# Kernel tuning notes

Measured on AMD Instinct MI355X. Metric: run time of the kernel, lower is better.

The kernel has to match this reference:

```python
import jax, jax.numpy as jnp
import numpy as np

SIZE = 1024      # codebook size
DIM = 64         # latent_dim
TOPK = 3
BETA_C = 0.25
LEGACY = False

def setup_inputs() -> dict:
    key = jax.random.key(0)
    kz, ke = jax.random.split(key)
    z = jax.random.normal(kz, (16, 64, 64, DIM), dtype=jnp.float32)
    # nn.Embedding init: uniform(-1/size, 1/size)
    emb = jax.random.uniform(ke, (SIZE, DIM), minval=-1.0 / SIZE, maxval=1.0 / SIZE, dtype=jnp.float32)
    return {"z": z, "emb": emb}

def reference(z, emb):
    zf = z.reshape(-1, DIM)                                  # [N, D]
    # squared euclidean distances via matmul expansion: [N, SIZE]
    d = (jnp.sum(zf ** 2, axis=1, keepdims=True)
         + jnp.sum(emb ** 2, axis=1)
         - 2.0 * (zf @ emb.T))
    neg_d, topk_idx = jax.lax.top_k(-d, TOPK)                # smallest distances -> [N, K]
    # direct gather instead of one-hot matmul (same math)
    z_q = jnp.mean(emb[topk_idx], axis=1).reshape(z.shape)   # [N,K,D] -> [N,D] -> z.shape
    if LEGACY:
        loss = (jnp.mean((jax.lax.stop_gradient(z_q) - z) ** 2)
                + BETA_C * jnp.mean((z_q - jax.lax.stop_gradient(z)) ** 2))
    else:
        loss = (BETA_C * jnp.mean((jax.lax.stop_gradient(z_q) - z) ** 2)
                + jnp.mean((z_q - jax.lax.stop_gradient(z)) ** 2))
    # one-hot encodings are part of the module's return signature
    topk_encodings = jax.nn.one_hot(topk_idx, SIZE, dtype=z.dtype)   # [N, K, SIZE]
    e_mean = jnp.mean(topk_encodings, axis=(0, 1))                   # [SIZE]
    perplexity = jnp.exp(-jnp.sum(e_mean * jnp.log(e_mean + 1e-10)))
    z_q_st = z + jax.lax.stop_gradient(z_q - z)              # straight-through estimator
    return (z_q_st, loss, perplexity, topk_encodings, topk_idx)
```

## Files before the change

### kernel.cpp

```cpp
#include <hip/hip_runtime.h>
#include <math.h>

#define N_ROWS 65536
#define CB 1024
#define SPLITS 4
#define JS (CB / SPLITS)

typedef float v4f __attribute__((ext_vector_type(4)));

__device__ __forceinline__ float tree_sum64_sq(const float* x) {
#pragma clang fp contract(off)
    float sq[64];
#pragma unroll
    for (int i = 0; i < 64; ++i) sq[i] = x[i] * x[i];
    float s[16];
#pragma unroll
    for (int l = 0; l < 16; ++l) s[l] = (sq[l] + sq[l + 16]) + (sq[l + 32] + sq[l + 48]);
    float t[8];
#pragma unroll
    for (int l = 0; l < 8; ++l) t[l] = s[l] + s[l + 8];
    float u[4];
#pragma unroll
    for (int l = 0; l < 4; ++l) u[l] = t[l] + t[l + 4];
    float v0 = u[0] + u[2];
    float v1 = u[1] + u[3];
    return v0 + v1;
}

__device__ __forceinline__ void top3_insert(float d, int j,
                                            float& v0, float& v1, float& v2,
                                            int& i0, int& i1, int& i2) {
    bool b0 = d < v0, b1 = d < v1, b2 = d < v2;
    v2 = b1 ? v1 : (b2 ? d : v2);
    i2 = b1 ? i1 : (b2 ? j : i2);
    v1 = b0 ? v0 : (b1 ? d : v1);
    i1 = b0 ? i0 : (b1 ? j : i1);
    v0 = b0 ? d : v0;
    i0 = b0 ? j : i0;
}

__global__ __launch_bounds__(256) void prep_kernel(const float* __restrict__ emb,
                                                   float* __restrict__ B,
                                                   int* __restrict__ hist,
                                                   float* __restrict__ lossAcc) {
    int j = blockIdx.x * 256 + threadIdx.x;
    if (j >= CB) return;
    float e[64];
    const float4* e4 = (const float4*)(emb + (size_t)j * 64);
#pragma unroll
    for (int k = 0; k < 16; ++k) {
        float4 v = e4[k];
        e[4 * k] = v.x; e[4 * k + 1] = v.y; e[4 * k + 2] = v.z; e[4 * k + 3] = v.w;
    }
    B[j] = tree_sum64_sq(e);
    hist[j] = 0;
    if (j == 0) *lossAcc = 0.0f;
}

__global__ __launch_bounds__(256) void fused_kernel(const float* __restrict__ z,
                                                    const float* __restrict__ emb,
                                                    const float* __restrict__ B,
                                                    float* __restrict__ out0,
                                                    float* __restrict__ out4,
                                                    int* __restrict__ hist,
                                                    float* __restrict__ lossAcc) {
    __shared__ float sD[SPLITS][64][3];
    __shared__ int   sI[SPLITS][64][3];

    int t = threadIdx.x;
    int r = t & 63;
    int split = __builtin_amdgcn_readfirstlane(t >> 6);
    int row = blockIdx.x * 64 + r;

    float zr[64];
    const float4* z4 = (const float4*)(z + (size_t)row * 64);
#pragma unroll
    for (int k = 0; k < 16; ++k) {
        float4 v = z4[k];
        zr[4 * k] = v.x; zr[4 * k + 1] = v.y; zr[4 * k + 2] = v.z; zr[4 * k + 3] = v.w;
    }
    float A = tree_sum64_sq(zr);

    float v0 = 3.402823466e38f, v1 = 3.402823466e38f, v2 = 3.402823466e38f;
    int i0 = 0, i1 = 0, i2 = 0;
    int jbase = split * JS;

    for (int jj = 0; jj < JS; ++jj) {
        int j = jbase + jj;
        const float4* e4 = (const float4*)(emb + (size_t)j * 64);
        float Bj = B[j];
        float acc = 0.0f;
#pragma unroll
        for (int k = 0; k < 16; ++k) {
            float4 e = e4[k];
            acc = fmaf(zr[4 * k],     e.x, acc);
            acc = fmaf(zr[4 * k + 1], e.y, acc);
            acc = fmaf(zr[4 * k + 2], e.z, acc);
            acc = fmaf(zr[4 * k + 3], e.w, acc);
        }
        float d = (A + Bj) - 2.0f * acc;
        top3_insert(d, j, v0, v1, v2, i0, i1, i2);
    }

    sD[split][r][0] = v0; sD[split][r][1] = v1; sD[split][r][2] = v2;
    sI[split][r][0] = i0; sI[split][r][1] = i1; sI[split][r][2] = i2;
    __syncthreads();

    if (t < 64) {
        float m0 = 3.402823466e38f, m1 = 3.402823466e38f, m2 = 3.402823466e38f;
        int j0 = 0, j1 = 0, j2 = 0;
#pragma unroll
        for (int s = 0; s < SPLITS; ++s) {
#pragma unroll
            for (int u = 0; u < 3; ++u)
                top3_insert(sD[s][r][u], sI[s][r][u], m0, m1, m2, j0, j1, j2);
        }

        const float4* e0q = (const float4*)(emb + (size_t)j0 * 64);
        const float4* e1q = (const float4*)(emb + (size_t)j1 * 64);
        const float4* e2q = (const float4*)(emb + (size_t)j2 * 64);
        v4f* o4 = (v4f*)(out0 + (size_t)row * 64);

        float lsum = 0.0f;
#pragma unroll
        for (int k4 = 0; k4 < 16; ++k4) {
            float4 a = e0q[k4], b = e1q[k4], c = e2q[k4];
            float zx = zr[4 * k4], zy = zr[4 * k4 + 1];
            float zz = zr[4 * k4 + 2], zw = zr[4 * k4 + 3];
            v4f st;
            float zq, df;
            zq = ((a.x + b.x) + c.x) / 3.0f; df = zq - zx; st.x = zx + df; lsum = fmaf(df, df, lsum);
            zq = ((a.y + b.y) + c.y) / 3.0f; df = zq - zy; st.y = zy + df; lsum = fmaf(df, df, lsum);
            zq = ((a.z + b.z) + c.z) / 3.0f; df = zq - zz; st.z = zz + df; lsum = fmaf(df, df, lsum);
            zq = ((a.w + b.w) + c.w) / 3.0f; df = zq - zw; st.w = zw + df; lsum = fmaf(df, df, lsum);
            __builtin_nontemporal_store(st, o4 + k4);
        }

        size_t ob = (size_t)row * 3;
        out4[ob]     = (float)j0;
        out4[ob + 1] = (float)j1;
        out4[ob + 2] = (float)j2;
        atomicAdd(&hist[j0], 1);
        atomicAdd(&hist[j1], 1);
        atomicAdd(&hist[j2], 1);

#pragma unroll
        for (int off = 32; off >= 1; off >>= 1) lsum += __shfl_down(lsum, off);
        if ((t & 63) == 0) atomicAdd(lossAcc, lsum);
    }
}

#define OH_GRID 2048
__global__ __launch_bounds__(256) void onehot_kernel(const float* __restrict__ idxf,
                                                     float* __restrict__ out3f) {
    v4f* o4 = (v4f*)(out3f + 2);
    const int M = (N_ROWS * 3 * CB - 2) / 4;
    const int stride = OH_GRID * 256;

    for (int m = blockIdx.x * 256 + threadIdx.x; m < M; m += stride) {
        int e0 = 2 + 4 * m;
        int s0 = e0 >> 10;
        int c0 = e0 & 1023;
        int s3 = (e0 + 3) >> 10;
        int ia = (int)idxf[s0];
        int ib = (int)idxf[s3];
        v4f v;
        v.x = (c0     == ia) ? 1.0f : 0.0f;
        v.y = (c0 + 1 == ia) ? 1.0f : 0.0f;
        v.z = (((c0 + 2) & 1023) == ib) ? 1.0f : 0.0f;
        v.w = (((c0 + 3) & 1023) == ib) ? 1.0f : 0.0f;
        __builtin_nontemporal_store(v, o4 + m);
    }

    if (blockIdx.x == 0 && threadIdx.x == 0) {
        int ia = (int)idxf[0];
        out3f[0] = (ia == 0) ? 1.0f : 0.0f;
        out3f[1] = (ia == 1) ? 1.0f : 0.0f;
        int ib = (int)idxf[N_ROWS * 3 - 1];
        out3f[(size_t)N_ROWS * 3 * CB - 2] = (ib == 1022) ? 1.0f : 0.0f;
        out3f[(size_t)N_ROWS * 3 * CB - 1] = (ib == 1023) ? 1.0f : 0.0f;
    }
}

__global__ __launch_bounds__(256) void finalize_kernel(const int* __restrict__ hist,
                                                       const float* __restrict__ lossAcc,
                                                       float* __restrict__ out1,
                                                       float* __restrict__ out2) {
    __shared__ float red[256];
    int t = threadIdx.x;
    float local = 0.0f;
    for (int b = t; b < CB; b += 256) {
        float em = (float)hist[b] / 196608.0f;
        local += em * logf(em + 1e-10f);
    }
    red[t] = local;
    __syncthreads();
    for (int s = 128; s >= 1; s >>= 1) {
        if (t < s) red[t] += red[t + s];
        __syncthreads();
    }
    if (t == 0) {
        *out2 = expf(-red[0]);
        float m = *lossAcc / 4194304.0f;
        *out1 = 0.25f * m + m;
    }
}

extern "C" void kernel_launch(void* const* d_in, const int* in_sizes, int n_in,
                              void* d_out, int out_size, void* d_ws, size_t ws_size,
                              hipStream_t stream) {
    const float* z   = (const float*)d_in[0];
    const float* emb = (const float*)d_in[1];

    float* out  = (float*)d_out;
    float* out0 = out;
    float* out1 = out + 4194304;
    float* out2 = out + 4194305;
    float* out3 = out + 4194306;
    float* out4 = out + 4194306 + 201326592ll;

    int*   hist    = (int*)d_ws;
    float* lossAcc = (float*)((char*)d_ws + 4096);
    float* B       = (float*)((char*)d_ws + 8192);

    prep_kernel<<<4, 256, 0, stream>>>(emb, B, hist, lossAcc);
    fused_kernel<<<N_ROWS / 64, 256, 0, stream>>>(z, emb, B, out0, out4,
                                                  hist, lossAcc);
    onehot_kernel<<<OH_GRID, 256, 0, stream>>>(out4, out3);
    finalize_kernel<<<1, 256, 0, stream>>>(hist, lossAcc, out1, out2);
}
```

Measured before the change: 1.082 ms.

## Fuse one-hot encoding write into distance kernel via LDS top-k indices

Removes the separate one-hot kernel and has each fused block write its own 64 rows of one-hot encodings, using top-k indices staged in shared memory instead of re-reading the float index output from global memory. This saves a kernel launch and the index reloads, and lets the large one-hot store stream overlap with distance computation in other blocks. It also adds an unroll-2 pragma on the codebook loop. The trade-off is that each block now finishes with a long store phase, which may change occupancy and scheduling.

```diff
diff --git a/kernel.cpp b/kernel.cpp
--- a/kernel.cpp
+++ b/kernel.cpp
@@ -61,11 +61,13 @@
                                                     const float* __restrict__ emb,
                                                     const float* __restrict__ B,
                                                     float* __restrict__ out0,
+                                                    float* __restrict__ out3f,
                                                     float* __restrict__ out4,
                                                     int* __restrict__ hist,
                                                     float* __restrict__ lossAcc) {
     __shared__ float sD[SPLITS][64][3];
     __shared__ int   sI[SPLITS][64][3];
+    __shared__ int   topk_lds[192];
 
     int t = threadIdx.x;
     int r = t & 63;
@@ -85,6 +87,7 @@
     int i0 = 0, i1 = 0, i2 = 0;
     int jbase = split * JS;
 
+#pragma unroll 2
     for (int jj = 0; jj < JS; ++jj) {
         int j = jbase + jj;
         const float4* e4 = (const float4*)(emb + (size_t)j * 64);
@@ -115,6 +118,10 @@
             for (int u = 0; u < 3; ++u)
                 top3_insert(sD[s][r][u], sI[s][r][u], m0, m1, m2, j0, j1, j2);
         }
+
+        topk_lds[r * 3]     = j0;
+        topk_lds[r * 3 + 1] = j1;
+        topk_lds[r * 3 + 2] = j2;
 
         const float4* e0q = (const float4*)(emb + (size_t)j0 * 64);
         const float4* e1q = (const float4*)(emb + (size_t)j1 * 64);
@@ -148,37 +155,33 @@
         for (int off = 32; off >= 1; off >>= 1) lsum += __shfl_down(lsum, off);
         if ((t & 63) == 0) atomicAdd(lossAcc, lsum);
     }
-}
-
-#define OH_GRID 2048
-__global__ __launch_bounds__(256) void onehot_kernel(const float* __restrict__ idxf,
-                                                     float* __restrict__ out3f) {
-    v4f* o4 = (v4f*)(out3f + 2);
-    const int M = (N_ROWS * 3 * CB - 2) / 4;
-    const int stride = OH_GRID * 256;
-
-    for (int m = blockIdx.x * 256 + threadIdx.x; m < M; m += stride) {
-        int e0 = 2 + 4 * m;
-        int s0 = e0 >> 10;
-        int c0 = e0 & 1023;
-        int s3 = (e0 + 3) >> 10;
-        int ia = (int)idxf[s0];
-        int ib = (int)idxf[s3];
+    __syncthreads();
+
+    float* Rb = out3f + (size_t)blockIdx.x * 196608;
+    v4f* R4 = (v4f*)(Rb + 2);
+    const int M = (196608 - 2) / 4;
+
+    for (int m = t; m < M; m += 256) {
+        int e  = 2 + 4 * m;
+        int s0 = e >> 10;
+        int c  = e & 1023;
+        int s3 = (e + 3) >> 10;
+        int ia = topk_lds[s0];
+        int ib = topk_lds[s3];
         v4f v;
-        v.x = (c0     == ia) ? 1.0f : 0.0f;
-        v.y = (c0 + 1 == ia) ? 1.0f : 0.0f;
-        v.z = (((c0 + 2) & 1023) == ib) ? 1.0f : 0.0f;
-        v.w = (((c0 + 3) & 1023) == ib) ? 1.0f : 0.0f;
-        __builtin_nontemporal_store(v, o4 + m);
-    }
-
-    if (blockIdx.x == 0 && threadIdx.x == 0) {
-        int ia = (int)idxf[0];
-        out3f[0] = (ia == 0) ? 1.0f : 0.0f;
-        out3f[1] = (ia == 1) ? 1.0f : 0.0f;
-        int ib = (int)idxf[N_ROWS * 3 - 1];
-        out3f[(size_t)N_ROWS * 3 * CB - 2] = (ib == 1022) ? 1.0f : 0.0f;
-        out3f[(size_t)N_ROWS * 3 * CB - 1] = (ib == 1023) ? 1.0f : 0.0f;
+        v.x = (c     == ia) ? 1.0f : 0.0f;
+        v.y = (c + 1 == ia) ? 1.0f : 0.0f;
+        v.z = (((c + 2) & 1023) == ib) ? 1.0f : 0.0f;
+        v.w = (((c + 3) & 1023) == ib) ? 1.0f : 0.0f;
+        __builtin_nontemporal_store(v, R4 + m);
+    }
+    if (t == 0) {
+        int ia = topk_lds[0];
+        Rb[0] = (ia == 0) ? 1.0f : 0.0f;
+        Rb[1] = (ia == 1) ? 1.0f : 0.0f;
+        int ib = topk_lds[191];
+        Rb[196606] = (ib == 1022) ? 1.0f : 0.0f;
+        Rb[196607] = (ib == 1023) ? 1.0f : 0.0f;
     }
 }
 
@@ -224,8 +227,7 @@
     float* B       = (float*)((char*)d_ws + 8192);
 
     prep_kernel<<<4, 256, 0, stream>>>(emb, B, hist, lossAcc);
-    fused_kernel<<<N_ROWS / 64, 256, 0, stream>>>(z, emb, B, out0, out4,
+    fused_kernel<<<N_ROWS / 64, 256, 0, stream>>>(z, emb, B, out0, out3, out4,
                                                   hist, lossAcc);
-    onehot_kernel<<<OH_GRID, 256, 0, stream>>>(out4, out3);
     finalize_kernel<<<1, 256, 0, stream>>>(hist, lossAcc, out1, out2);
 }
```

Result: faster. 1.061 ms (-2.0%).
